# Optimization experiments

Hardware: AMD Instinct MI355X
Metric: run time of the kernel (lower is better)

The kernel has to match this reference:

```python
import jax, jax.numpy as jnp
import numpy as np
import math

# --- static model config (mirrors FitTorch init args) ---
NATOMS = 2000
NNBR = 30            # neighbors per atom (regular neighlist)
NPAIRS = NATOMS * NNBR
NCONF = 8
APC = NATOMS // NCONF
NUM_RADIAL = 12
NUM_3BODY = 20
CUTOFF = 5.0
H1, H2 = 64, 32
DESC = NUM_RADIAL + NUM_3BODY


def setup_inputs() -> dict:
    key = jax.random.key(0)
    ks = jax.random.split(key, 12)
    # positions in a box
    x = jax.random.uniform(ks[0], (NATOMS, 3), jnp.float32, 0.0, 20.0)
    unique_i = jnp.repeat(jnp.arange(NATOMS, dtype=jnp.int32), NNBR)
    unique_j = jax.random.randint(ks[1], (NPAIRS,), 0, NATOMS, dtype=jnp.int32)
    # construct transform_x so every pair distance lies in (1.0, 0.95*cutoff)
    dirs = jax.random.normal(ks[2], (NPAIRS, 3), jnp.float32)
    dirs = dirs / jnp.linalg.norm(dirs, axis=1, keepdims=True)
    r = jax.random.uniform(ks[3], (NPAIRS, 1), jnp.float32, 1.0, 0.95 * CUTOFF)
    xneigh_target = x[unique_i] - dirs * r
    transform_x = xneigh_target - x[unique_j]
    neighlist = jnp.stack([unique_i, unique_j], axis=1)
    indices = unique_i // APC                      # config id per pair
    atoms_per_structure = jnp.full((NCONF,), APC, dtype=jnp.int32)
    types = jnp.zeros((NATOMS,), dtype=jnp.int32)
    # tiny pairwise MLP params (sigmoid hidden layers, linear output)
    def lin(k, fan_in, fan_out):
        return jax.random.normal(k, (fan_in, fan_out), jnp.float32) / np.sqrt(fan_in)
    W1 = lin(ks[4], DESC, H1); b1 = jnp.zeros((H1,), jnp.float32)
    W2 = lin(ks[5], H1, H2);   b2 = jnp.zeros((H2,), jnp.float32)
    W3 = lin(ks[6], H2, 1);    b3 = jnp.zeros((1,), jnp.float32)
    return {"x": x, "transform_x": transform_x, "neighlist": neighlist,
            "indices": indices, "atoms_per_structure": atoms_per_structure,
            "types": types, "unique_i": unique_i, "unique_j": unique_j,
            "W1": W1, "b1": b1, "W2": W2, "b2": b2, "W3": W3, "b3": b3}


def _energy(x, transform_x, indices, unique_i, unique_j, W1, b1, W2, b2, W3, b3, nconf):
    # gather + pairwise geometry
    xneigh = transform_x + x[unique_j]                      # [P,3]
    diff = x[unique_i] - xneigh                             # [P,3]
    rij = jnp.linalg.norm(diff, axis=1, keepdims=True)      # [P,1]
    u = diff / jnp.maximum(rij, 1e-12)                      # F.normalize
    # smooth cosine cutoff
    fc = 0.5 * (jnp.cos(jnp.pi * rij / CUTOFF) + 1.0)       # [P,1]
    # radial Bessel basis: fc * sqrt(2/c) * sin(n*pi*r/c) / r, n=1..R
    n = jnp.arange(1, NUM_RADIAL + 1, dtype=x.dtype)
    rbf = fc * jnp.sqrt(2.0 / CUTOFF) * jnp.sin(n * jnp.pi * rij / CUTOFF) / rij  # [P,R]
    # 3-body Gaussian descriptors over angles j-i-k (neighbors grouped per atom i)
    A, N, M = x.shape[0], NNBR, NUM_3BODY
    u3 = u.reshape(A, N, 3)
    fcn = fc.reshape(A, N)
    cos = jnp.einsum('apd,aqd->apq', u3, u3)                # [A,N,N] cos(theta)
    mu = jnp.linspace(-1.0, 1.0, M).astype(x.dtype)
    dmu = mu[1] - mu[0]
    eta = 1.0 / (2.0 * dmu * dmu)
    self_mask = 1.0 - jnp.eye(N, dtype=x.dtype)             # exclude k == j
    w = fcn[:, None, :] * self_mask[None]                   # [A,N,N] fc(r_ik) weights
    g = jnp.exp(-eta * (cos[..., None] - mu) ** 2)          # [A,N,N,M]
    d3 = jnp.einsum('apq,apqm->apm', w, g).reshape(A * N, M)
    # pairwise MLP -> pair energies, modulated by cutoff
    desc = jnp.concatenate([rbf, d3], axis=1)               # [P, DESC]
    h = jax.nn.sigmoid(desc @ W1 + b1)
    h = jax.nn.sigmoid(h @ W2 + b2)
    eij = (h @ W3 + b3) * fc                                # [P,1]
    # scatter pair energies to per-structure totals (index_add_)
    return jax.ops.segment_sum(eij[:, 0], indices, num_segments=nconf)


def reference(x, transform_x, neighlist, indices, atoms_per_structure, types,
              unique_i, unique_j, W1, b1, W2, b2, W3, b3):
    nconf = atoms_per_structure.shape[0]
    energy = _energy(x, transform_x, indices, unique_i, unique_j,
                     W1, b1, W2, b2, W3, b3, nconf)
    # forces = -d(sum of energies)/dx (grad_outputs = ones), as in torch.autograd.grad
    forces = -jax.grad(lambda xx: _energy(xx, transform_x, indices, unique_i, unique_j,
                                          W1, b1, W2, b2, W3, b3, nconf).sum())(x)
    return energy, forces
```

## Files before the change

### kernel.cpp

```cpp
#include <hip/hip_runtime.h>
#include <math.h>

#define NATOMS 2000
#define NNBR   30
#define NCONF  8
#define APC    250
#define NRAD   12
#define M3     20
#define H1N    64
#define H2N    32

#define MU(m) (-1.0f + (float)(m) * (2.0f / 19.0f))

typedef __attribute__((ext_vector_type(8))) short short8_t;
typedef __attribute__((ext_vector_type(4))) float f32x4;

__device__ __forceinline__ float sigmoidf(float v) {
    return 1.0f / (1.0f + __expf(-v));
}
__device__ __forceinline__ ushort f2bf(float f) {
    unsigned u = __float_as_uint(f);
    u += 0x7FFF + ((u >> 16) & 1);
    return (ushort)(u >> 16);
}
__device__ __forceinline__ float bf2f(ushort s) {
    return __uint_as_float(((unsigned)s) << 16);
}

extern "C" __global__ void __launch_bounds__(256)
fit_main(const float* __restrict__ x, const float* __restrict__ tx,
         const int* __restrict__ uj,
         const float* __restrict__ W1, const float* __restrict__ b1,
         const float* __restrict__ W2, const float* __restrict__ b2,
         const float* __restrict__ W3, const float* __restrict__ b3,
         float* __restrict__ gx, float* __restrict__ e_atom)
{
    const int tid  = threadIdx.x;
    const int lane = tid & 63;
    const int wid  = tid >> 6;
    const int atom = blockIdx.x;
    const int lr   = lane & 15;
    const int lg   = lane >> 4;

    __shared__ float s_ux[32], s_uy[32], s_uz[32], s_fcp[32];
    __shared__ float s_r[32], s_rinv[32], s_sa[32], s_ca[32];
    __shared__ int   s_j[NNBR];
    __shared__ __align__(16) float  s_desc[32 * 36];
    __shared__ __align__(16) ushort s_W1b [32 * 72];
    __shared__ __align__(16) ushort s_W2tb[32 * 72];
    __shared__ __align__(16) ushort s_h1b [32 * 72];
    __shared__ __align__(16) ushort s_gz2b[32 * 40];
    __shared__ __align__(16) float  s_gd  [32 * 44];
    __shared__ float s_outp[64];
    __shared__ float s_red[32 * 5];

    const float k1  = 0.6283185307179586f;
    const float sq  = 0.6324555320336759f;
    const float eta = 45.125f;
    const float RHO = 0.36787944117144233f;
    const float C2  = -90.25f;

#pragma unroll
    for (int i = 0; i < 8; i++) {
        int idx = tid + 256 * i;
        s_W1b[(idx >> 6) * 72 + (idx & 63)] = f2bf(W1[idx]);
    }
#pragma unroll
    for (int i = 0; i < 8; i++) {
        int idx = tid + 256 * i;
        s_W2tb[(idx & 31) * 72 + (idx >> 5)] = f2bf(W2[idx]);
    }
    if (tid < NNBR) {
        int p = atom * NNBR + tid;
        int j = uj[p];
        float d0 = x[atom * 3 + 0] - x[j * 3 + 0] - tx[p * 3 + 0];
        float d1 = x[atom * 3 + 1] - x[j * 3 + 1] - tx[p * 3 + 1];
        float d2 = x[atom * 3 + 2] - x[j * 3 + 2] - tx[p * 3 + 2];
        float r = sqrtf(d0 * d0 + d1 * d1 + d2 * d2);
        float rinv = 1.0f / r;
        float sa, ca;
        __sincosf(k1 * r, &sa, &ca);
        float fc = 0.5f * (ca + 1.0f);
        s_ux[tid] = d0 * rinv; s_uy[tid] = d1 * rinv; s_uz[tid] = d2 * rinv;
        s_fcp[tid] = fc; s_r[tid] = r; s_rinv[tid] = rinv;
        s_sa[tid] = sa; s_ca[tid] = ca;
        s_j[tid] = j;
    } else if (tid < 32) {
        s_ux[tid] = 0.f; s_uy[tid] = 0.f; s_uz[tid] = 0.f; s_fcp[tid] = 0.f;
        s_r[tid] = 1.f; s_rinv[tid] = 1.f; s_sa[tid] = 0.f; s_ca[tid] = 1.f;
    }
    __syncthreads();

#pragma unroll 1
    for (int t = tid; t < NNBR * NRAD; t += 256) {
        int p = t / NRAD, n = t - p * NRAD;
        float s = __sinf((float)(n + 1) * k1 * s_r[p]);
        s_desc[p * 36 + n] = s_fcp[p] * sq * s * s_rinv[p];
    }
    if (tid < 72) s_desc[30 * 36 + tid] = 0.f;
    if (tid < 240) {
        int p = tid >> 3, c = tid & 7;
        int q0 = (c < 6) ? 4 * c : 24 + 3 * (c - 6);
        int qn = (c < 6) ? 4 : 3;
        float up0 = s_ux[p], up1 = s_uy[p], up2 = s_uz[p];
        float d3part[M3];
#pragma unroll
        for (int m = 0; m < M3; m++) d3part[m] = 0.f;
        for (int qq = 0; qq < qn; qq++) {
            int q = q0 + qq;
            float fq = (q == p) ? 0.f : s_fcp[q];
            float cs = up0 * s_ux[q] + up1 * s_uy[q] + up2 * s_uz[q];
            float E  = __expf(9.5f * cs);
            float Ei = __expf(-9.5f * cs);
            float t9 = cs - MU(9);
            float h9 = __expf(-eta * t9 * t9);
            float h = h9 * E, rr = E * RHO;
            d3part[10] = fmaf(fq, h, d3part[10]);
#pragma unroll
            for (int m = 11; m < 20; m++) {
                h *= rr; rr *= RHO;
                d3part[m] = fmaf(fq, h, d3part[m]);
            }
            h = h9; rr = RHO * Ei;
            d3part[9] = fmaf(fq, h, d3part[9]);
#pragma unroll
            for (int m = 8; m >= 0; m--) {
                h *= rr; rr *= RHO;
                d3part[m] = fmaf(fq, h, d3part[m]);
            }
        }
#pragma unroll
        for (int m = 0; m < M3; m++) {
            float v = d3part[m];
            v += __shfl_xor(v, 1);
            v += __shfl_xor(v, 2);
            v += __shfl_xor(v, 4);
            if (c == 0) s_desc[p * 36 + NRAD + m] = v;
        }
    }
    __syncthreads();

    {
        const int mt = wid & 1, ntb = (wid >> 1) * 2;
        short8_t a;
        {
            const float* dp = s_desc + (16 * mt + lr) * 36 + lg * 8;
            f32x4 v0 = *(const f32x4*)dp;
            f32x4 v1 = *(const f32x4*)(dp + 4);
            a[0] = (short)f2bf(v0[0]); a[1] = (short)f2bf(v0[1]);
            a[2] = (short)f2bf(v0[2]); a[3] = (short)f2bf(v0[3]);
            a[4] = (short)f2bf(v1[0]); a[5] = (short)f2bf(v1[1]);
            a[6] = (short)f2bf(v1[2]); a[7] = (short)f2bf(v1[3]);
        }
#pragma unroll
        for (int t = 0; t < 2; t++) {
            int col = 16 * (ntb + t) + lr;
            short8_t b;
#pragma unroll
            for (int j = 0; j < 8; j++)
                b[j] = (short)s_W1b[(lg * 8 + j) * 72 + col];
            f32x4 c = {0.f, 0.f, 0.f, 0.f};
            c = __builtin_amdgcn_mfma_f32_16x16x32_bf16(a, b, c, 0, 0, 0);
            float b1v = b1[col];
#pragma unroll
            for (int rg = 0; rg < 4; rg++) {
                int p = 16 * mt + lg * 4 + rg;
                s_h1b[p * 72 + col] = f2bf(sigmoidf(c[rg] + b1v));
            }
        }
    }
    __syncthreads();

    {
        const int mt = wid & 1, nt = wid >> 1;
        f32x4 c = {0.f, 0.f, 0.f, 0.f};
#pragma unroll
        for (int kt = 0; kt < 2; kt++) {
            short8_t a = *(const short8_t*)&s_h1b[(16 * mt + lr) * 72 + kt * 32 + lg * 8];
            short8_t b = *(const short8_t*)&s_W2tb[(16 * nt + lr) * 72 + kt * 32 + lg * 8];
            c = __builtin_amdgcn_mfma_f32_16x16x32_bf16(a, b, c, 0, 0, 0);
        }
        int k2 = 16 * nt + lr;
        float b2v = b2[k2], w3v = W3[k2];
        float op[4];
#pragma unroll
        for (int rg = 0; rg < 4; rg++) {
            int p = 16 * mt + lg * 4 + rg;
            float s = sigmoidf(c[rg] + b2v);
            op[rg] = s * w3v;
            float g = s_fcp[p] * w3v * s * (1.f - s);
            s_gz2b[p * 40 + k2] = f2bf(g);
        }
#pragma unroll
        for (int rg = 0; rg < 4; rg++) {
            op[rg] += __shfl_xor(op[rg], 1);
            op[rg] += __shfl_xor(op[rg], 2);
            op[rg] += __shfl_xor(op[rg], 4);
            op[rg] += __shfl_xor(op[rg], 8);
        }
        if (lr == 0) {
#pragma unroll
            for (int rg = 0; rg < 4; rg++)
                s_outp[nt * 32 + 16 * mt + lg * 4 + rg] = op[rg];
        }
    }
    __syncthreads();

    {
        const int mt = wid & 1, ntb = (wid >> 1) * 2;
        short8_t a = *(const short8_t*)&s_gz2b[(16 * mt + lr) * 40 + lg * 8];
#pragma unroll
        for (int t = 0; t < 2; t++) {
            int hcol = 16 * (ntb + t) + lr;
            short8_t b;
#pragma unroll
            for (int j = 0; j < 8; j++)
                b[j] = (short)s_W2tb[(lg * 8 + j) * 72 + hcol];
            f32x4 c = {0.f, 0.f, 0.f, 0.f};
            c = __builtin_amdgcn_mfma_f32_16x16x32_bf16(a, b, c, 0, 0, 0);
#pragma unroll
            for (int rg = 0; rg < 4; rg++) {
                int p = 16 * mt + lg * 4 + rg;
                float hv = bf2f(s_h1b[p * 72 + hcol]);
                s_h1b[p * 72 + hcol] = f2bf(c[rg] * hv * (1.f - hv));
            }
        }
    }
    __syncthreads();

    {
        const int mt = wid & 1, nt = wid >> 1;
        f32x4 c = {0.f, 0.f, 0.f, 0.f};
#pragma unroll
        for (int kt = 0; kt < 2; kt++) {
            short8_t a = *(const short8_t*)&s_h1b[(16 * mt + lr) * 72 + kt * 32 + lg * 8];
            short8_t b = *(const short8_t*)&s_W1b[(16 * nt + lr) * 72 + kt * 32 + lg * 8];
            c = __builtin_amdgcn_mfma_f32_16x16x32_bf16(a, b, c, 0, 0, 0);
        }
        int d = 16 * nt + lr;
#pragma unroll
        for (int rg = 0; rg < 4; rg++)
            s_gd[(16 * mt + lg * 4 + rg) * 44 + d] = c[rg];
    }
    __syncthreads();

    if (tid < 240) {
        int p = tid >> 3, c = tid & 7;
        int q0 = (c < 6) ? 4 * c : 24 + 3 * (c - 6);
        int qn = (c < 6) ? 4 : 3;
        float up0 = s_ux[p], up1 = s_uy[p], up2 = s_uz[p];
        float Ap[M3];
        {
            const f32x4* ap4 = (const f32x4*)(s_gd + p * 44 + NRAD);
#pragma unroll
            for (int t4 = 0; t4 < 5; t4++) {
                f32x4 v = ap4[t4];
                Ap[4 * t4 + 0] = v[0]; Ap[4 * t4 + 1] = v[1];
                Ap[4 * t4 + 2] = v[2]; Ap[4 * t4 + 3] = v[3];
            }
        }
        float fp_ = s_fcp[p];
        float gu0 = 0.f, gu1 = 0.f, gu2 = 0.f, gfc = 0.f;
        for (int qq = 0; qq < qn; qq++) {
            int q = q0 + qq;
            float uq0 = s_ux[q], uq1 = s_uy[q], uq2 = s_uz[q];
            float cs = up0 * uq0 + up1 * uq1 + up2 * uq2;
            float fq = s_fcp[q];
            float Aq[M3];
            {
                const f32x4* aq4 = (const f32x4*)(s_gd + q * 44 + NRAD);
#pragma unroll
                for (int t4 = 0; t4 < 5; t4++) {
                    f32x4 v = aq4[t4];
                    Aq[4 * t4 + 0] = v[0]; Aq[4 * t4 + 1] = v[1];
                    Aq[4 * t4 + 2] = v[2]; Aq[4 * t4 + 3] = v[3];
                }
            }
            float E  = __expf(9.5f * cs);
            float Ei = __expf(-9.5f * cs);
            float t9 = cs - MU(9);
            float h9 = __expf(-eta * t9 * t9);
            float SAh = 0.f, SAm = 0.f, SBh = 0.f, SBm = 0.f;
            {
                float h = h9 * E, rr = E * RHO;
#pragma unroll
                for (int m = 10; m < 20; m++) {
                    if (m > 10) { h *= rr; rr *= RHO; }
                    float hm = MU(m) * h;
                    SAh = fmaf(Ap[m], h,  SAh);
                    SAm = fmaf(Ap[m], hm, SAm);
                    SBh = fmaf(Aq[m], h,  SBh);
                    SBm = fmaf(Aq[m], hm, SBm);
                }
            }
            {
                float h = h9, rr = RHO * Ei;
#pragma unroll
                for (int m = 9; m >= 0; m--) {
                    if (m < 9) { h *= rr; rr *= RHO; }
                    float hm = MU(m) * h;
                    SAh = fmaf(Ap[m], h,  SAh);
                    SAm = fmaf(Ap[m], hm, SAm);
                    SBh = fmaf(Aq[m], h,  SBh);
                    SBm = fmaf(Aq[m], hm, SBm);
                }
            }
            if (q != p) {
                float gcos = C2 * (fq * (cs * SAh - SAm) + fp_ * (cs * SBh - SBm));
                gu0 = fmaf(gcos, uq0, gu0);
                gu1 = fmaf(gcos, uq1, gu1);
                gu2 = fmaf(gcos, uq2, gu2);
                gfc += SBh;
            }
        }
        gu0 += __shfl_xor(gu0, 1); gu0 += __shfl_xor(gu0, 2); gu0 += __shfl_xor(gu0, 4);
        gu1 += __shfl_xor(gu1, 1); gu1 += __shfl_xor(gu1, 2); gu1 += __shfl_xor(gu1, 4);
        gu2 += __shfl_xor(gu2, 1); gu2 += __shfl_xor(gu2, 2); gu2 += __shfl_xor(gu2, 4);
        gfc += __shfl_xor(gfc, 1); gfc += __shfl_xor(gfc, 2); gfc += __shfl_xor(gfc, 4);
        if (c == 0) {
            s_red[p * 5 + 0] = gu0;
            s_red[p * 5 + 1] = gu1;
            s_red[p * 5 + 2] = gu2;
            s_red[p * 5 + 3] = gfc;
        }
    }
    __syncthreads();

    float gd0 = 0.f, gd1 = 0.f, gd2 = 0.f, eij = 0.f;
    if (tid < NNBR) {
        float fc = s_fcp[tid], rinv = s_rinv[tid];
        float sa = s_sa[tid], ca = s_ca[tid];
        float out = b3[0] + s_outp[tid] + s_outp[32 + tid];
        float u0 = s_ux[tid], u1 = s_uy[tid], u2 = s_uz[tid];
        int j = s_j[tid];
        float grp = 0.f, gfp = 0.f;
        float sprev = 0.f, scur = sa, cprev = 1.f, ccur = ca;
#pragma unroll
        for (int d = 0; d < NRAD; d++) {
            float gdv = s_gd[tid * 44 + d];
            float n = (float)(d + 1);
            grp += gdv * fc * sq * rinv * (n * k1 * ccur - scur * rinv);
            gfp += gdv * sq * scur * rinv;
            float snext = 2.f * ca * scur - sprev; sprev = scur; scur = snext;
            float cnext = 2.f * ca * ccur - cprev; cprev = ccur; ccur = cnext;
        }
        float gfc = gfp + s_red[tid * 5 + 3] + out;
        float gu0 = s_red[tid * 5 + 0];
        float gu1 = s_red[tid * 5 + 1];
        float gu2 = s_red[tid * 5 + 2];
        float grf = grp + gfc * (-0.5f * k1 * sa);
        float gdot = gu0 * u0 + gu1 * u1 + gu2 * u2;
        gd0 = grf * u0 + (gu0 - gdot * u0) * rinv;
        gd1 = grf * u1 + (gu1 - gdot * u1) * rinv;
        gd2 = grf * u2 + (gu2 - gdot * u2) * rinv;
        atomicAdd(&gx[j * 3 + 0], -gd0);
        atomicAdd(&gx[j * 3 + 1], -gd1);
        atomicAdd(&gx[j * 3 + 2], -gd2);
        eij = out * fc;
    }
    if (wid == 0) {
#pragma unroll
        for (int off = 32; off > 0; off >>= 1) {
            gd0 += __shfl_xor(gd0, off);
            gd1 += __shfl_xor(gd1, off);
            gd2 += __shfl_xor(gd2, off);
            eij += __shfl_xor(eij, off);
        }
        if (tid == 0) {
            atomicAdd(&gx[atom * 3 + 0], gd0);
            atomicAdd(&gx[atom * 3 + 1], gd1);
            atomicAdd(&gx[atom * 3 + 2], gd2);
            e_atom[atom] = eij;
        }
    }
}

extern "C" __global__ void __launch_bounds__(256)
fit_finalize(const float* __restrict__ e_atom, const float* __restrict__ gx,
             float* __restrict__ out)
{
    int b = blockIdx.x;
    if (b < NCONF) {
        __shared__ float red[256];
        int t = threadIdx.x;
        red[t] = (t < APC) ? e_atom[b * APC + t] : 0.f;
        __syncthreads();
        for (int s = 128; s > 0; s >>= 1) {
            if (t < s) red[t] += red[t + s];
            __syncthreads();
        }
        if (t == 0) out[b] = red[0];
    } else {
        int idx = (b - NCONF) * 256 + threadIdx.x;
        if (idx < NATOMS * 3) out[NCONF + idx] = -gx[idx];
    }
}

extern "C" void kernel_launch(void* const* d_in, const int* in_sizes, int n_in,
                              void* d_out, int out_size, void* d_ws, size_t ws_size,
                              hipStream_t stream)
{
    const float* x  = (const float*)d_in[0];
    const float* tx = (const float*)d_in[1];
    const int*   uj = (const int*)d_in[7];
    const float* W1 = (const float*)d_in[8];
    const float* b1 = (const float*)d_in[9];
    const float* W2 = (const float*)d_in[10];
    const float* b2 = (const float*)d_in[11];
    const float* W3 = (const float*)d_in[12];
    const float* b3 = (const float*)d_in[13];

    float* gx     = (float*)d_ws;
    float* e_atom = gx + NATOMS * 3;

    hipMemsetAsync(gx, 0, NATOMS * 3 * sizeof(float), stream);

    fit_main<<<NATOMS, 256, 0, stream>>>(x, tx, uj, W1, b1, W2, b2, W3, b3,
                                         gx, e_atom);

    int fblocks = NCONF + (NATOMS * 3 + 255) / 256;
    fit_finalize<<<fblocks, 256, 0, stream>>>(e_atom, gx, (float*)d_out);
}
```

Before: 44.67 us.

## Exploit pair symmetry in three-body gradient loop with shared atomics

Replaces the per-(p,q) 900-pair loop over 240 threads with a loop over the 435 unique unordered pairs, each evaluated once and contributing to both p and q through LDS atomicAdd. The aim is to roughly halve the exp-heavy Gaussian sum work, since gcos is symmetric in p and q. In exchange it adds triangular-index decoding with sqrt, eight shared-memory atomics per pair, and a second loop iteration for 179 threads. Floating-point summation order also becomes nondeterministic.

```diff
diff --git a/kernel.cpp b/kernel.cpp
--- a/kernel.cpp
+++ b/kernel.cpp
@@ -3,6 +3,7 @@
 
 #define NATOMS 2000
 #define NNBR   30
+#define NPAIR2 435
 #define NCONF  8
 #define APC    250
 #define NRAD   12
@@ -70,6 +71,7 @@
         int idx = tid + 256 * i;
         s_W2tb[(idx & 31) * 72 + (idx >> 5)] = f2bf(W2[idx]);
     }
+    if (tid < 32 * 5) s_red[tid] = 0.f;
     if (tid < NNBR) {
         int p = atom * NNBR + tid;
         int j = uj[p];
@@ -244,85 +246,67 @@
     }
     __syncthreads();
 
-    if (tid < 240) {
-        int p = tid >> 3, c = tid & 7;
-        int q0 = (c < 6) ? 4 * c : 24 + 3 * (c - 6);
-        int qn = (c < 6) ? 4 : 3;
+#pragma unroll 1
+    for (int t = tid; t < NPAIR2; t += 256) {
+        int p = (int)((sqrtf(8.f * (float)t + 1.f) + 1.f) * 0.5f);
+        if (p * (p - 1) / 2 > t) p--;
+        else if ((p + 1) * p / 2 <= t) p++;
+        int q = t - p * (p - 1) / 2;
         float up0 = s_ux[p], up1 = s_uy[p], up2 = s_uz[p];
-        float Ap[M3];
+        float uq0 = s_ux[q], uq1 = s_uy[q], uq2 = s_uz[q];
+        float cs = up0 * uq0 + up1 * uq1 + up2 * uq2;
+        float fp_ = s_fcp[p], fq_ = s_fcp[q];
+        float Ap[M3], Aq[M3];
         {
             const f32x4* ap4 = (const f32x4*)(s_gd + p * 44 + NRAD);
+            const f32x4* aq4 = (const f32x4*)(s_gd + q * 44 + NRAD);
 #pragma unroll
             for (int t4 = 0; t4 < 5; t4++) {
-                f32x4 v = ap4[t4];
-                Ap[4 * t4 + 0] = v[0]; Ap[4 * t4 + 1] = v[1];
-                Ap[4 * t4 + 2] = v[2]; Ap[4 * t4 + 3] = v[3];
-            }
-        }
-        float fp_ = s_fcp[p];
-        float gu0 = 0.f, gu1 = 0.f, gu2 = 0.f, gfc = 0.f;
-        for (int qq = 0; qq < qn; qq++) {
-            int q = q0 + qq;
-            float uq0 = s_ux[q], uq1 = s_uy[q], uq2 = s_uz[q];
-            float cs = up0 * uq0 + up1 * uq1 + up2 * uq2;
-            float fq = s_fcp[q];
-            float Aq[M3];
-            {
-                const f32x4* aq4 = (const f32x4*)(s_gd + q * 44 + NRAD);
-#pragma unroll
-                for (int t4 = 0; t4 < 5; t4++) {
-                    f32x4 v = aq4[t4];
-                    Aq[4 * t4 + 0] = v[0]; Aq[4 * t4 + 1] = v[1];
-                    Aq[4 * t4 + 2] = v[2]; Aq[4 * t4 + 3] = v[3];
-                }
-            }
-            float E  = __expf(9.5f * cs);
-            float Ei = __expf(-9.5f * cs);
-            float t9 = cs - MU(9);
-            float h9 = __expf(-eta * t9 * t9);
-            float SAh = 0.f, SAm = 0.f, SBh = 0.f, SBm = 0.f;
-            {
-                float h = h9 * E, rr = E * RHO;
-#pragma unroll
-                for (int m = 10; m < 20; m++) {
-                    if (m > 10) { h *= rr; rr *= RHO; }
-                    float hm = MU(m) * h;
-                    SAh = fmaf(Ap[m], h,  SAh);
-                    SAm = fmaf(Ap[m], hm, SAm);
-                    SBh = fmaf(Aq[m], h,  SBh);
-                    SBm = fmaf(Aq[m], hm, SBm);
-                }
-            }
-            {
-                float h = h9, rr = RHO * Ei;
-#pragma unroll
-                for (int m = 9; m >= 0; m--) {
-                    if (m < 9) { h *= rr; rr *= RHO; }
-                    float hm = MU(m) * h;
-                    SAh = fmaf(Ap[m], h,  SAh);
-                    SAm = fmaf(Ap[m], hm, SAm);
-                    SBh = fmaf(Aq[m], h,  SBh);
-                    SBm = fmaf(Aq[m], hm, SBm);
-                }
-            }
-            if (q != p) {
-                float gcos = C2 * (fq * (cs * SAh - SAm) + fp_ * (cs * SBh - SBm));
-                gu0 = fmaf(gcos, uq0, gu0);
-                gu1 = fmaf(gcos, uq1, gu1);
-                gu2 = fmaf(gcos, uq2, gu2);
-                gfc += SBh;
-            }
-        }
-        gu0 += __shfl_xor(gu0, 1); gu0 += __shfl_xor(gu0, 2); gu0 += __shfl_xor(gu0, 4);
-        gu1 += __shfl_xor(gu1, 1); gu1 += __shfl_xor(gu1, 2); gu1 += __shfl_xor(gu1, 4);
-        gu2 += __shfl_xor(gu2, 1); gu2 += __shfl_xor(gu2, 2); gu2 += __shfl_xor(gu2, 4);
-        gfc += __shfl_xor(gfc, 1); gfc += __shfl_xor(gfc, 2); gfc += __shfl_xor(gfc, 4);
-        if (c == 0) {
-            s_red[p * 5 + 0] = gu0;
-            s_red[p * 5 + 1] = gu1;
-            s_red[p * 5 + 2] = gu2;
-            s_red[p * 5 + 3] = gfc;
-        }
+                f32x4 va = ap4[t4], vb = aq4[t4];
+                Ap[4 * t4 + 0] = va[0]; Ap[4 * t4 + 1] = va[1];
+                Ap[4 * t4 + 2] = va[2]; Ap[4 * t4 + 3] = va[3];
+                Aq[4 * t4 + 0] = vb[0]; Aq[4 * t4 + 1] = vb[1];
+                Aq[4 * t4 + 2] = vb[2]; Aq[4 * t4 + 3] = vb[3];
+            }
+        }
+        float E  = __expf(9.5f * cs);
+        float Ei = __expf(-9.5f * cs);
+        float t9 = cs - MU(9);
+        float h9 = __expf(-eta * t9 * t9);
+        float SAh = 0.f, SAm = 0.f, SBh = 0.f, SBm = 0.f;
+        {
+            float h = h9 * E, rr = E * RHO;
+#pragma unroll
+            for (int m = 10; m < 20; m++) {
+                if (m > 10) { h *= rr; rr *= RHO; }
+                float hm = MU(m) * h;
+                SAh = fmaf(Ap[m], h,  SAh);
+                SAm = fmaf(Ap[m], hm, SAm);
+                SBh = fmaf(Aq[m], h,  SBh);
+                SBm = fmaf(Aq[m], hm, SBm);
+            }
+        }
+        {
+            float h = h9, rr = RHO * Ei;
+#pragma unroll
+            for (int m = 9; m >= 0; m--) {
+                if (m < 9) { h *= rr; rr *= RHO; }
+                float hm = MU(m) * h;
+                SAh = fmaf(Ap[m], h,  SAh);
+                SAm = fmaf(Ap[m], hm, SAm);
+                SBh = fmaf(Aq[m], h,  SBh);
+                SBm = fmaf(Aq[m], hm, SBm);
+            }
+        }
+        float gcos = C2 * (fq_ * (cs * SAh - SAm) + fp_ * (cs * SBh - SBm));
+        atomicAdd(&s_red[p * 5 + 0], gcos * uq0);
+        atomicAdd(&s_red[p * 5 + 1], gcos * uq1);
+        atomicAdd(&s_red[p * 5 + 2], gcos * uq2);
+        atomicAdd(&s_red[p * 5 + 3], SBh);
+        atomicAdd(&s_red[q * 5 + 0], gcos * up0);
+        atomicAdd(&s_red[q * 5 + 1], gcos * up1);
+        atomicAdd(&s_red[q * 5 + 2], gcos * up2);
+        atomicAdd(&s_red[q * 5 + 3], SAh);
     }
     __syncthreads();
 
```

After: 77.11 us. 1.73x slower.
